# Performance work log

Measured on AMD Instinct MI355X. Metric: run time of the kernel, lower is better.

The kernel has to match this reference:

```python
import jax, jax.numpy as jnp
import numpy as np

H = 90            # hidden_size (hard-coded in module)
NODE_F = 16       # conv1 in_channels = dim(x) + dim(pos)
EDGE_F = 8
N_GRAPHS = 512


def _init_linear(key, fan_in, fan_out):
    kw, kb = jax.random.split(key)
    bound = 1.0 / np.sqrt(fan_in)
    w = jax.random.uniform(kw, (fan_in, fan_out), minval=-bound, maxval=bound, dtype=jnp.float32)
    b = jax.random.uniform(kb, (fan_out,), minval=-bound, maxval=bound, dtype=jnp.float32)
    return w, b


def setup_inputs() -> dict:
    key = jax.random.key(0)
    ks = jax.random.split(key, 16)
    N, E = 16000, 64000
    x = jax.random.normal(ks[0], (N, 13), dtype=jnp.float32)
    pos = jax.random.normal(ks[1], (N, 3), dtype=jnp.float32)
    edge_attr = jax.random.normal(ks[2], (E, EDGE_F), dtype=jnp.float32)
    edge_index = jax.random.randint(ks[3], (2, E), 0, N, dtype=jnp.int32)
    batch = jnp.sort(jax.random.randint(ks[4], (N,), 0, N_GRAPHS, dtype=jnp.int32))

    # conv1: edge MLP edge_f -> H -> NODE_F*H ; root [NODE_F,H]; bias [H]
    c1_w1, c1_b1 = _init_linear(ks[5], EDGE_F, H)
    c1_w2, c1_b2 = _init_linear(ks[6], H, NODE_F * H)
    c1_root = jax.random.normal(ks[7], (NODE_F, H), dtype=jnp.float32) / np.sqrt(NODE_F)
    c1_bias = jnp.zeros((H,), dtype=jnp.float32)
    # conv2: H -> H
    c2_w1, c2_b1 = _init_linear(ks[8], EDGE_F, H)
    c2_w2, c2_b2 = _init_linear(ks[9], H, H * H)
    c2_root = jax.random.normal(ks[10], (H, H), dtype=jnp.float32) / np.sqrt(H)
    c2_bias = jnp.zeros((H,), dtype=jnp.float32)
    # conv3: H -> H//2
    c3_w1, c3_b1 = _init_linear(ks[11], EDGE_F, H)
    c3_w2, c3_b2 = _init_linear(ks[12], H, H * (H // 2))
    c3_root = jax.random.normal(ks[13], (H, H // 2), dtype=jnp.float32) / np.sqrt(H)
    c3_bias = jnp.zeros((H // 2,), dtype=jnp.float32)

    fc1_w, fc1_b = _init_linear(ks[14], H // 2, H)
    out_w, out_b = _init_linear(ks[15], H, 1)

    return dict(x=x, pos=pos, edge_attr=edge_attr, edge_index=edge_index, batch=batch,
                c1_w1=c1_w1, c1_b1=c1_b1, c1_w2=c1_w2, c1_b2=c1_b2, c1_root=c1_root, c1_bias=c1_bias,
                c2_w1=c2_w1, c2_b1=c2_b1, c2_w2=c2_w2, c2_b2=c2_b2, c2_root=c2_root, c2_bias=c2_bias,
                c3_w1=c3_w1, c3_b1=c3_b1, c3_w2=c3_w2, c3_b2=c3_b2, c3_root=c3_root, c3_bias=c3_bias,
                fc1_w=fc1_w, fc1_b=fc1_b, out_w=out_w, out_b=out_b)


def _nnconv(x, src, dst, edge_attr, w1, b1, w2, b2, root, bias, in_c, out_c):
    # edge MLP -> per-edge weight matrix theta[e] in R^{in_c x out_c}
    h = jax.nn.relu(edge_attr @ w1 + b1)                  # [E, H]
    theta = (h @ w2 + b2).reshape(-1, in_c, out_c)        # [E, in_c, out_c]
    msg = jnp.einsum('ei,eio->eo', x[src], theta)         # gather + per-edge matvec
    agg = jax.ops.segment_sum(msg, dst, num_segments=x.shape[0])  # scatter-add
    return agg + x @ root + bias


def reference(x, pos, edge_attr, edge_index, batch,
              c1_w1, c1_b1, c1_w2, c1_b2, c1_root, c1_bias,
              c2_w1, c2_b1, c2_w2, c2_b2, c2_root, c2_bias,
              c3_w1, c3_b1, c3_w2, c3_b2, c3_root, c3_bias,
              fc1_w, fc1_b, out_w, out_b):
    src, dst = edge_index[0], edge_index[1]
    h = jnp.concatenate([x, pos], axis=1)                 # [N, NODE_F]
    h = jax.nn.relu(_nnconv(h, src, dst, edge_attr, c1_w1, c1_b1, c1_w2, c1_b2, c1_root, c1_bias, NODE_F, H))
    h = jax.nn.relu(_nnconv(h, src, dst, edge_attr, c2_w1, c2_b1, c2_w2, c2_b2, c2_root, c2_bias, H, H))
    h = jax.nn.relu(_nnconv(h, src, dst, edge_attr, c3_w1, c3_b1, c3_w2, c3_b2, c3_root, c3_bias, H, H // 2))
    g = jax.ops.segment_sum(h, batch, num_segments=N_GRAPHS)  # global_add_pool
    g = jax.nn.relu(g @ fc1_w + fc1_b)
    return g @ out_w + out_b                               # [N_GRAPHS, 1]
```

## Files before the change

### kernel.cpp

```cpp
#include <hip/hip_runtime.h>

#define NN 16000
#define NE 64000
#define HD 90
#define NG 512

typedef float f32x4 __attribute__((ext_vector_type(4)));
typedef short s16x8 __attribute__((ext_vector_type(8)));

__device__ __forceinline__ unsigned short rhu1(float f) {
  return (unsigned short)((__builtin_bit_cast(unsigned int, f) + 0x8000u) >> 16);
}
__device__ __forceinline__ unsigned int rhu_pack(float lo, float hi) {
  unsigned int ul = __builtin_bit_cast(unsigned int, lo) + 0x8000u;
  unsigned int uh = __builtin_bit_cast(unsigned int, hi) + 0x8000u;
  return __builtin_amdgcn_perm(uh, ul, 0x07060302u);
}
__device__ __forceinline__ float bfhi(unsigned int u) {
  return __builtin_bit_cast(float, u & 0xFFFF0000u);
}
__device__ __forceinline__ float bflo(unsigned int u) {
  return __builtin_bit_cast(float, u << 16);
}

__global__ void concat_kernel(const float* __restrict__ x, const float* __restrict__ pos,
                              float* __restrict__ h0) {
  int idx = blockIdx.x * 256 + threadIdx.x;
  if (idx >= NN * 16) return;
  int n = idx >> 4, c = idx & 15;
  h0[idx] = (c < 13) ? x[n * 13 + c] : pos[n * 3 + (c - 13)];
}

__global__ void edge_mlp_bf(const float* __restrict__ ea, const float* __restrict__ w1,
                            const float* __restrict__ b1, unsigned short* __restrict__ he) {
  int idx = blockIdx.x * 256 + threadIdx.x;
  if (idx >= NE * 96) return;
  int e = idx / 96, k = idx - e * 96;
  unsigned short v;
  if (k < 90) {
    const float* a = ea + e * 8;
    float acc = b1[k];
#pragma unroll
    for (int j = 0; j < 8; j++) acc = fmaf(a[j], w1[j * HD + k], acc);
    v = rhu1(fmaxf(acc, 0.f));
  } else {
    v = (k == 90) ? (unsigned short)0x3F80 : (unsigned short)0;
  }
  he[idx] = v;
}

template <int OC, int NTT>
__global__ void wprep_frag(const float* __restrict__ w2, const float* __restrict__ b2,
                           unsigned short* __restrict__ wout, int inc_oc) {
  const int i = blockIdx.x / 3, c = blockIdx.x - 3 * (blockIdx.x / 3);
  __shared__ float t_s[32 * 100];
  const int tid = threadIdx.x;
  for (int idx = tid; idx < 32 * 96; idx += 256) {
    int kk = idx / 96, o = idx - kk * 96;
    int hk = c * 32 + kk;
    float v = 0.f;
    if (o < OC) {
      if (hk < 90) v = w2[hk * inc_oc + i * OC + o];
      else if (hk == 90) v = b2[i * OC + o];
    }
    t_s[kk * 100 + o] = v;
  }
  __syncthreads();
  unsigned int* wo = (unsigned int*)(wout + (size_t)i * NTT * 3 * 512) + c * 256;
  for (int idx = tid; idx < NTT * 256; idx += 256) {
    int t = idx >> 8, r = idx & 255;
    int lane = r >> 2, u = r & 3;
    int kk = (lane >> 4) * 8 + 2 * u;
    int o = t * 16 + (lane & 15);
    wo[(size_t)t * 3 * 256 + lane * 4 + u] = rhu_pack(t_s[kk * 100 + o], t_s[(kk + 1) * 100 + o]);
  }
}

template <int ILIM, int OC, int NTT, int NWG, int MT, int EPB, int BLK>
__global__ __launch_bounds__(BLK, 2)
void msg_mfma(const unsigned short* __restrict__ he,
              const float* __restrict__ nin,
              const int* __restrict__ src, const int* __restrict__ dst,
              const unsigned short* __restrict__ wp,
              float* __restrict__ agg) {
  constexpr int WMG = EPB / 32;
  constexpr int TPE = BLK / EPB;
  constexpr int NWAVES = BLK / 64;
  constexpr int NF = NTT * 3;
  constexpr int MG = MT / 2;
  __shared__ unsigned short zb[ILIM * WMG * 32];
  __shared__ unsigned short wbA[NF * 512];
  __shared__ unsigned short wbB[NF * 512];
  __shared__ int dst_s[EPB];
  const int tid = threadIdx.x;
  const int e0 = blockIdx.x * EPB;
  const int wid = tid >> 6, l = tid & 63, ln = tid & 15, q = (tid & 63) >> 4;
  const int wn = wid % NWG, wm = wid / NWG;
  const int eb = wm * MT * 16;
  const int wn3 = wn * 3;

  const unsigned short* wl = wp + l * 8;
  auto stage = [&](const unsigned short* wb, unsigned short* lb) {
#pragma unroll
    for (int t = 0; t < (NF + NWAVES - 1) / NWAVES; t++) {
      const int s = wid + t * NWAVES;
      if (s < NF) {
        __builtin_amdgcn_global_load_lds(
            (const __attribute__((address_space(1))) unsigned int*)(wb + (size_t)s * 512),
            (__attribute__((address_space(3))) unsigned int*)(lb + s * 512),
            16, 0, 0);
      }
    }
  };

  f32x4 acc[MT][3];
  s16x8 af[MT][3];
  auto compute = [&](int i, const unsigned short* lb) {
    f32x4 zv[MT];
#pragma unroll
    for (int g = 0; g < MG; g++) {
      const uint4 zu = *(const uint4*)&zb[(i * WMG + wm * MG + g) * 32 + q * 8];
      zv[2 * g][0] = bflo(zu.x); zv[2 * g][1] = bfhi(zu.x);
      zv[2 * g][2] = bflo(zu.y); zv[2 * g][3] = bfhi(zu.y);
      zv[2 * g + 1][0] = bflo(zu.z); zv[2 * g + 1][1] = bfhi(zu.z);
      zv[2 * g + 1][2] = bflo(zu.w); zv[2 * g + 1][3] = bfhi(zu.w);
    }
    uint4 ba[9];
#pragma unroll
    for (int ntl = 0; ntl < 3; ntl++)
#pragma unroll
      for (int c = 0; c < 3; c++)
        ba[ntl * 3 + c] = *(const uint4*)(lb + ((wn3 + ntl) * 3 + c) * 512 + l * 8);
#pragma unroll
    for (int ntl = 0; ntl < 3; ntl++) {
#pragma unroll
      for (int mt = 0; mt < MT; mt++) {
        f32x4 t = __builtin_amdgcn_mfma_f32_16x16x32_bf16(af[mt][0], __builtin_bit_cast(s16x8, ba[ntl * 3 + 0]), (f32x4)0.f, 0, 0, 0);
        t = __builtin_amdgcn_mfma_f32_16x16x32_bf16(af[mt][1], __builtin_bit_cast(s16x8, ba[ntl * 3 + 1]), t, 0, 0, 0);
        t = __builtin_amdgcn_mfma_f32_16x16x32_bf16(af[mt][2], __builtin_bit_cast(s16x8, ba[ntl * 3 + 2]), t, 0, 0, 0);
        acc[mt][ntl] += zv[mt] * t;
      }
    }
  };

  stage(wl, wbA);

  if (tid < EPB) dst_s[tid] = dst[e0 + tid];

  {
    const int e = tid % EPB, jj = tid / EPB;
    const int base = (e >> 5) * 32 + (((e & 15) >> 2) << 3) + (((e >> 4) & 1) << 2) + (e & 3);
    const float* zr = nin + (size_t)src[e0 + e] * ILIM;
    for (int p = jj; p < ILIM / 2; p += TPE) {
      const float2 v = *(const float2*)(zr + 2 * p);
      zb[(2 * p) * (WMG * 32) + base] = rhu1(v.x);
      zb[(2 * p + 1) * (WMG * 32) + base] = rhu1(v.y);
    }
  }

#pragma unroll
  for (int mt = 0; mt < MT; mt++) {
    const unsigned short* hr = he + (size_t)(e0 + eb + mt * 16 + ln) * 96 + q * 8;
#pragma unroll
    for (int c = 0; c < 3; c++) af[mt][c] = *(const s16x8*)(hr + c * 32);
  }

#pragma unroll
  for (int mt = 0; mt < MT; mt++)
#pragma unroll
    for (int nt = 0; nt < 3; nt++) acc[mt][nt] = (f32x4)0.f;

  __syncthreads();

  const unsigned short* wnext = wl + (size_t)NF * 512;

#pragma clang loop unroll(disable)
  for (int i = 0; i < ILIM; i += 2) {
    stage(wnext, wbB);
    wnext += (size_t)NF * 512;
    compute(i, wbA);
    __syncthreads();
    if (i + 2 < ILIM) {
      stage(wnext, wbA);
      wnext += (size_t)NF * 512;
    }
    compute(i + 1, wbB);
    if (i + 2 < ILIM) __syncthreads();
  }

#pragma unroll
  for (int mt = 0; mt < MT; mt++) {
#pragma unroll
    for (int ntl = 0; ntl < 3; ntl++) {
      int o = wn * 48 + ntl * 16 + ln;
      if (o < OC) {
#pragma unroll
        for (int r = 0; r < 4; r++) {
          int el = eb + mt * 16 + q * 4 + r;
          atomicAdd(agg + (size_t)dst_s[el] * OC + o, acc[mt][ntl][r]);
        }
      }
    }
  }
}

template <int IN_C, int OC>
__global__ void node_kernel(const float* __restrict__ agg, const float* __restrict__ nin,
                            const float* __restrict__ root, const float* __restrict__ bias,
                            float* __restrict__ out) {
  int idx = blockIdx.x * 256 + threadIdx.x;
  if (idx >= NN * OC) return;
  int n = idx / OC, o = idx - n * OC;
  float acc = agg[idx] + bias[o];
  const float* inp = nin + (size_t)n * IN_C;
#pragma unroll 6
  for (int i = 0; i < IN_C; i++) acc = fmaf(inp[i], root[i * OC + o], acc);
  out[idx] = fmaxf(acc, 0.f);
}

__global__ void pool_mlp_kernel(const float* __restrict__ h3, const int* __restrict__ batch,
                                const float* __restrict__ fc1_w, const float* __restrict__ fc1_b,
                                const float* __restrict__ out_w, const float* __restrict__ out_b,
                                float* __restrict__ out) {
  const int b = blockIdx.x;
  const int tid = threadIdx.x;
  __shared__ float g[45];
  __shared__ float go[90];
  __shared__ int rng[2];
  if (tid < 2) {
    int target = b + tid;
    int lo = 0, hi = NN;
    while (lo < hi) { int mid = (lo + hi) >> 1; if (batch[mid] < target) lo = mid + 1; else hi = mid; }
    rng[tid] = lo;
  }
  __syncthreads();
  const int s = rng[0], e = rng[1];
  if (tid < 45) {
    float acc = 0.f;
    for (int n = s; n < e; n++) acc += h3[n * 45 + tid];
    g[tid] = acc;
  }
  __syncthreads();
  if (tid < 90) {
    float acc = fc1_b[tid];
#pragma unroll 5
    for (int i = 0; i < 45; i++) acc = fmaf(g[i], fc1_w[i * 90 + tid], acc);
    go[tid] = fmaxf(acc, 0.f) * out_w[tid];
  }
  __syncthreads();
  if (tid == 0) {
    float acc = out_b[0];
    for (int i = 0; i < 90; i++) acc += go[i];
    out[b] = acc;
  }
}

extern "C" void kernel_launch(void* const* d_in, const int* in_sizes, int n_in,
                              void* d_out, int out_size, void* d_ws, size_t ws_size,
                              hipStream_t stream) {
  const float* x       = (const float*)d_in[0];
  const float* pos     = (const float*)d_in[1];
  const float* ea      = (const float*)d_in[2];
  const int*   eidx    = (const int*)d_in[3];
  const int*   batch   = (const int*)d_in[4];
  const float* c1_w1   = (const float*)d_in[5];
  const float* c1_b1   = (const float*)d_in[6];
  const float* c1_w2   = (const float*)d_in[7];
  const float* c1_b2   = (const float*)d_in[8];
  const float* c1_root = (const float*)d_in[9];
  const float* c1_bias = (const float*)d_in[10];
  const float* c2_w1   = (const float*)d_in[11];
  const float* c2_b1   = (const float*)d_in[12];
  const float* c2_w2   = (const float*)d_in[13];
  const float* c2_b2   = (const float*)d_in[14];
  const float* c2_root = (const float*)d_in[15];
  const float* c2_bias = (const float*)d_in[16];
  const float* c3_w1   = (const float*)d_in[17];
  const float* c3_b1   = (const float*)d_in[18];
  const float* c3_w2   = (const float*)d_in[19];
  const float* c3_b2   = (const float*)d_in[20];
  const float* c3_root = (const float*)d_in[21];
  const float* c3_bias = (const float*)d_in[22];
  const float* fc1_w   = (const float*)d_in[23];
  const float* fc1_b   = (const float*)d_in[24];
  const float* out_w   = (const float*)d_in[25];
  const float* out_b   = (const float*)d_in[26];
  const int* src = eidx;
  const int* dst = eidx + NE;

  float* ws  = (float*)d_ws;
  float* h0  = ws;
  float* h1  = h0 + NN * 16;
  float* h2  = h1 + NN * 90;
  float* h3  = h2 + NN * 90;
  float* agg = h3 + NN * 45;
  unsigned short* he_bf = (unsigned short*)(agg + NN * 90);
  unsigned short* wp1 = he_bf + (size_t)NE * 96;
  unsigned short* wp2 = wp1 + (size_t)16 * 6 * 3 * 512;
  unsigned short* wp3 = wp2 + (size_t)90 * 6 * 3 * 512;

  concat_kernel<<<(NN * 16) / 256, 256, 0, stream>>>(x, pos, h0);

  wprep_frag<90, 6><<<16 * 3, 256, 0, stream>>>(c1_w2, c1_b2, wp1, 16 * 90);
  wprep_frag<90, 6><<<90 * 3, 256, 0, stream>>>(c2_w2, c2_b2, wp2, 90 * 90);
  wprep_frag<45, 3><<<90 * 3, 256, 0, stream>>>(c3_w2, c3_b2, wp3, 90 * 45);

  hipMemsetAsync(agg, 0, (size_t)NN * 90 * sizeof(float), stream);
  edge_mlp_bf<<<(NE * 96) / 256, 256, 0, stream>>>(ea, c1_w1, c1_b1, he_bf);
  msg_mfma<16, 90, 6, 2, 4, 256, 512><<<NE / 256, 512, 0, stream>>>(he_bf, h0, src, dst, wp1, agg);
  node_kernel<16, 90><<<(NN * 90) / 256, 256, 0, stream>>>(agg, h0, c1_root, c1_bias, h1);

  hipMemsetAsync(agg, 0, (size_t)NN * 90 * sizeof(float), stream);
  edge_mlp_bf<<<(NE * 96) / 256, 256, 0, stream>>>(ea, c2_w1, c2_b1, he_bf);
  msg_mfma<90, 90, 6, 2, 4, 128, 256><<<NE / 128, 256, 0, stream>>>(he_bf, h1, src, dst, wp2, agg);
  node_kernel<90, 90><<<(NN * 90) / 256, 256, 0, stream>>>(agg, h1, c2_root, c2_bias, h2);

  hipMemsetAsync(agg, 0, (size_t)NN * 45 * sizeof(float), stream);
  edge_mlp_bf<<<(NE * 96) / 256, 256, 0, stream>>>(ea, c3_w1, c3_b1, he_bf);
  msg_mfma<90, 45, 3, 1, 4, 256, 256><<<NE / 256, 256, 0, stream>>>(he_bf, h2, src, dst, wp3, agg);
  node_kernel<90, 45><<<(NN * 45 + 255) / 256, 256, 0, stream>>>(agg, h2, c3_root, c3_bias, h3);

  pool_mlp_kernel<<<NG, 128, 0, stream>>>(h3, batch, fc1_w, fc1_b, out_w, out_b, (float*)d_out);
}
```

Baseline: 529.8 us.

## Fuse edge MLP into message kernel and fold agg zeroing into node kernel

Each message kernel now computes the edge-MLP hidden activations (bf16, with the bias column appended) straight into its MFMA A-fragments from edge_attr and w1. This removes the separate edge_mlp kernels and the round trip through the bf16 edge buffer in global memory. The node kernel clears agg after reading it, so the memsets between layers are no longer needed. Layer 2 also moves to 256 edges per 512-thread block. The cost is recomputing the MLP inside every wave column group, and the node kernel passes the same pointer as two __restrict__ arguments.

Measured after the change: 761.6 us. 43.8% more time.

```diff
diff --git a/kernel.cpp b/kernel.cpp
--- a/kernel.cpp
+++ b/kernel.cpp
@@ -29,24 +29,6 @@
   if (idx >= NN * 16) return;
   int n = idx >> 4, c = idx & 15;
   h0[idx] = (c < 13) ? x[n * 13 + c] : pos[n * 3 + (c - 13)];
-}
-
-__global__ void edge_mlp_bf(const float* __restrict__ ea, const float* __restrict__ w1,
-                            const float* __restrict__ b1, unsigned short* __restrict__ he) {
-  int idx = blockIdx.x * 256 + threadIdx.x;
-  if (idx >= NE * 96) return;
-  int e = idx / 96, k = idx - e * 96;
-  unsigned short v;
-  if (k < 90) {
-    const float* a = ea + e * 8;
-    float acc = b1[k];
-#pragma unroll
-    for (int j = 0; j < 8; j++) acc = fmaf(a[j], w1[j * HD + k], acc);
-    v = rhu1(fmaxf(acc, 0.f));
-  } else {
-    v = (k == 90) ? (unsigned short)0x3F80 : (unsigned short)0;
-  }
-  he[idx] = v;
 }
 
 template <int OC, int NTT>
@@ -78,7 +60,8 @@
 
 template <int ILIM, int OC, int NTT, int NWG, int MT, int EPB, int BLK>
 __global__ __launch_bounds__(BLK, 2)
-void msg_mfma(const unsigned short* __restrict__ he,
+void msg_mfma(const float* __restrict__ ea,
+              const float* __restrict__ w1, const float* __restrict__ b1,
               const float* __restrict__ nin,
               const int* __restrict__ src, const int* __restrict__ dst,
               const unsigned short* __restrict__ wp,
@@ -160,9 +143,34 @@
 
 #pragma unroll
   for (int mt = 0; mt < MT; mt++) {
-    const unsigned short* hr = he + (size_t)(e0 + eb + mt * 16 + ln) * 96 + q * 8;
-#pragma unroll
-    for (int c = 0; c < 3; c++) af[mt][c] = *(const s16x8*)(hr + c * 32);
+    const float* a = ea + (size_t)(e0 + eb + mt * 16 + ln) * 8;
+    const float a0 = a[0], a1 = a[1], a2 = a[2], a3 = a[3];
+    const float a4 = a[4], a5 = a[5], a6 = a[6], a7 = a[7];
+#pragma unroll
+    for (int c = 0; c < 3; c++) {
+      s16x8 v;
+#pragma unroll
+      for (int j = 0; j < 8; j++) {
+        const int k = c * 32 + q * 8 + j;
+        unsigned short hv;
+        if (k < 90) {
+          float s = b1[k];
+          s = fmaf(a0, w1[0 * HD + k], s);
+          s = fmaf(a1, w1[1 * HD + k], s);
+          s = fmaf(a2, w1[2 * HD + k], s);
+          s = fmaf(a3, w1[3 * HD + k], s);
+          s = fmaf(a4, w1[4 * HD + k], s);
+          s = fmaf(a5, w1[5 * HD + k], s);
+          s = fmaf(a6, w1[6 * HD + k], s);
+          s = fmaf(a7, w1[7 * HD + k], s);
+          hv = rhu1(fmaxf(s, 0.f));
+        } else {
+          hv = (k == 90) ? (unsigned short)0x3F80 : (unsigned short)0;
+        }
+        v[j] = (short)hv;
+      }
+      af[mt][c] = v;
+    }
   }
 
 #pragma unroll
@@ -205,13 +213,15 @@
 }
 
 template <int IN_C, int OC>
-__global__ void node_kernel(const float* __restrict__ agg, const float* __restrict__ nin,
+__global__ void node_kernel(const float* __restrict__ agg_r, float* __restrict__ agg,
+                            const float* __restrict__ nin,
                             const float* __restrict__ root, const float* __restrict__ bias,
                             float* __restrict__ out) {
   int idx = blockIdx.x * 256 + threadIdx.x;
   if (idx >= NN * OC) return;
   int n = idx / OC, o = idx - n * OC;
-  float acc = agg[idx] + bias[o];
+  float acc = agg_r[idx] + bias[o];
+  agg[idx] = 0.f;
   const float* inp = nin + (size_t)n * IN_C;
 #pragma unroll 6
   for (int i = 0; i < IN_C; i++) acc = fmaf(inp[i], root[i * OC + o], acc);
@@ -294,8 +304,7 @@
   float* h2  = h1 + NN * 90;
   float* h3  = h2 + NN * 90;
   float* agg = h3 + NN * 45;
-  unsigned short* he_bf = (unsigned short*)(agg + NN * 90);
-  unsigned short* wp1 = he_bf + (size_t)NE * 96;
+  unsigned short* wp1 = (unsigned short*)(agg + NN * 90);
   unsigned short* wp2 = wp1 + (size_t)16 * 6 * 3 * 512;
   unsigned short* wp3 = wp2 + (size_t)90 * 6 * 3 * 512;
 
@@ -306,19 +315,14 @@
   wprep_frag<45, 3><<<90 * 3, 256, 0, stream>>>(c3_w2, c3_b2, wp3, 90 * 45);
 
   hipMemsetAsync(agg, 0, (size_t)NN * 90 * sizeof(float), stream);
-  edge_mlp_bf<<<(NE * 96) / 256, 256, 0, stream>>>(ea, c1_w1, c1_b1, he_bf);
-  msg_mfma<16, 90, 6, 2, 4, 256, 512><<<NE / 256, 512, 0, stream>>>(he_bf, h0, src, dst, wp1, agg);
-  node_kernel<16, 90><<<(NN * 90) / 256, 256, 0, stream>>>(agg, h0, c1_root, c1_bias, h1);
-
-  hipMemsetAsync(agg, 0, (size_t)NN * 90 * sizeof(float), stream);
-  edge_mlp_bf<<<(NE * 96) / 256, 256, 0, stream>>>(ea, c2_w1, c2_b1, he_bf);
-  msg_mfma<90, 90, 6, 2, 4, 128, 256><<<NE / 128, 256, 0, stream>>>(he_bf, h1, src, dst, wp2, agg);
-  node_kernel<90, 90><<<(NN * 90) / 256, 256, 0, stream>>>(agg, h1, c2_root, c2_bias, h2);
-
-  hipMemsetAsync(agg, 0, (size_t)NN * 45 * sizeof(float), stream);
-  edge_mlp_bf<<<(NE * 96) / 256, 256, 0, stream>>>(ea, c3_w1, c3_b1, he_bf);
-  msg_mfma<90, 45, 3, 1, 4, 256, 256><<<NE / 256, 256, 0, stream>>>(he_bf, h2, src, dst, wp3, agg);
-  node_kernel<90, 45><<<(NN * 45 + 255) / 256, 256, 0, stream>>>(agg, h2, c3_root, c3_bias, h3);
+  msg_mfma<16, 90, 6, 2, 4, 256, 512><<<NE / 256, 512, 0, stream>>>(ea, c1_w1, c1_b1, h0, src, dst, wp1, agg);
+  node_kernel<16, 90><<<(NN * 90) / 256, 256, 0, stream>>>(agg, agg, h0, c1_root, c1_bias, h1);
+
+  msg_mfma<90, 90, 6, 2, 4, 256, 512><<<NE / 256, 512, 0, stream>>>(ea, c2_w1, c2_b1, h1, src, dst, wp2, agg);
+  node_kernel<90, 90><<<(NN * 90) / 256, 256, 0, stream>>>(agg, agg, h1, c2_root, c2_bias, h2);
+
+  msg_mfma<90, 45, 3, 1, 4, 256, 256><<<NE / 256, 256, 0, stream>>>(ea, c3_w1, c3_b1, h2, src, dst, wp3, agg);
+  node_kernel<90, 45><<<(NN * 45 + 255) / 256, 256, 0, stream>>>(agg, agg, h2, c3_root, c3_bias, h3);
 
   pool_mlp_kernel<<<NG, 128, 0, stream>>>(h3, batch, fc1_w, fc1_b, out_w, out_b, (float*)d_out);
 }
```
